# Kernel optimization log

Measured on AMD Instinct MI355X. Metric: run time of the kernel, lower is better.

The kernel has to match this reference:

```python
import jax, jax.numpy as jnp
import numpy as np

H = 16
MAX_LEN = 150
NEG_INF = -1e30  # stand-in for -inf that is fp16-safe after cast; matches masked_fill(-inf) semantics


def setup_inputs() -> dict:
    key = jax.random.key(0)
    ks = jax.random.split(key, 12)
    B, L, D = 4, 1024, 1024
    Dh = D // H
    Q = jax.random.normal(ks[0], (B, L, D), jnp.float32)
    K = jax.random.normal(ks[1], (B, L, D), jnp.float32)
    V = jax.random.normal(ks[2], (B, L, D), jnp.float32)
    # boolean mask, True = masked out; keep diagonal unmasked to avoid fully-masked rows
    mask = jax.random.bernoulli(ks[3], 0.3, (B, L, L))
    mask = jnp.logical_and(mask, ~jnp.eye(L, dtype=bool)[None])
    s = 0.02
    Wq = jax.random.normal(ks[4], (D, D), jnp.float32) * s
    Wk = jax.random.normal(ks[5], (D, D), jnp.float32) * s
    Wv = jax.random.normal(ks[6], (D, D), jnp.float32) * s
    Wo = jax.random.normal(ks[7], (D, D), jnp.float32) * s
    bq = jax.random.normal(ks[8], (D,), jnp.float32) * s
    bk = jax.random.normal(ks[9], (D,), jnp.float32) * s
    bv = jax.random.normal(ks[10], (D,), jnp.float32) * s
    bo = jax.random.normal(ks[11], (D,), jnp.float32) * s
    pos_emb = jnp.zeros((2 * MAX_LEN + 1, Dh), jnp.float32)  # nn.Parameter(torch.zeros(...))
    # perturb so the bias path is exercised
    pos_emb = pos_emb + jax.random.normal(jax.random.fold_in(key, 99), pos_emb.shape, jnp.float32) * s
    return {"Q": Q, "K": K, "V": V, "mask": mask,
            "Wq": Wq, "bq": bq, "Wk": Wk, "bk": bk, "Wv": Wv, "bv": bv,
            "Wo": Wo, "bo": bo, "pos_emb": pos_emb}


def _mha_relative(Q, K, V, mask, Wq, bq, Wk, bk, Wv, bv, Wo, bo, pos_emb):
    B, Lq, D = Q.shape
    Lk = K.shape[1]
    Dh = D // H
    # torch nn.Linear: y = x @ W.T + b
    q = (Q @ Wq.T + bq).reshape(B, Lq, H, Dh).transpose(0, 2, 1, 3)  # [B,H,Lq,Dh]
    k = (K @ Wk.T + bk).reshape(B, Lk, H, Dh).transpose(0, 2, 1, 3)
    v = (V @ Wv.T + bv).reshape(B, Lk, H, Dh).transpose(0, 2, 1, 3)
    # relative position indices, replicating torch's negative-index wraparound via mod
    rel = jnp.arange(Lk)[None, :] - jnp.arange(Lq)[:, None]
    rel = jnp.clip(rel, -MAX_LEN, MAX_LEN)
    idx = (rel + MAX_LEN - 1) % (2 * MAX_LEN + 1)  # torch pos_embedding[-1] == row 2*max_len
    Rtab = pos_emb[idx]                            # [Lq,Lk,Dh]
    Rp = jnp.einsum('bhqd,qkd->bhqk', q, Rtab)     # relative-position bias
    scores = (jnp.einsum('bhqd,bhkd->bhqk', q, k) + Rp) / jnp.sqrt(jnp.float32(Dh))
    scores = jnp.where(mask[:, None], NEG_INF, scores)
    p = jax.nn.softmax(scores, axis=-1)
    attn = jnp.einsum('bhqk,bhkd->bhqd', p, v)     # [B,H,Lq,Dh]
    attn = attn.transpose(0, 2, 1, 3).reshape(B, Lq, D)
    return attn @ Wo.T + bo                        # dropout is identity in eval


def reference(Q, K, V, mask, Wq, bq, Wk, bk, Wv, bv, Wo, bo, pos_emb):
    return _mha_relative(Q, K, V, mask, Wq, bq, Wk, bk, Wv, bv, Wo, bo, pos_emb)
```

## Files before the change

### kernel.cpp

```cpp
#include <hip/hip_runtime.h>
#include <hip/hip_bf16.h>

#define BB 4
#define LL 1024
#define DD 1024
#define HH 16
#define DH 64
#define NPOS 301
#define MAXL 150
#define NEG_INF -1e30f

typedef __attribute__((ext_vector_type(4))) float f32x4;
typedef __attribute__((ext_vector_type(8))) short short8;

__device__ inline unsigned short f2b(float x) {
    __hip_bfloat16 h = __float2bfloat16(x);
    return *reinterpret_cast<unsigned short*>(&h);
}
__device__ inline unsigned pack2(float a, float b) {
    return (unsigned)f2b(a) | ((unsigned)f2b(b) << 16);
}
__device__ inline float b2f(unsigned short u) {
    return __uint_as_float((unsigned)u << 16);
}

template <bool F32>
__device__ inline short8 ld8(const void* p, size_t off) {
    if constexpr (F32) {
        const float* q = (const float*)p + off;
        float4 a = *reinterpret_cast<const float4*>(q);
        float4 b = *reinterpret_cast<const float4*>(q + 4);
        short8 r;
        r[0] = (short)f2b(a.x); r[1] = (short)f2b(a.y);
        r[2] = (short)f2b(a.z); r[3] = (short)f2b(a.w);
        r[4] = (short)f2b(b.x); r[5] = (short)f2b(b.y);
        r[6] = (short)f2b(b.z); r[7] = (short)f2b(b.w);
        return r;
    } else {
        return *reinterpret_cast<const short8*>((const unsigned short*)p + off);
    }
}

__global__ __launch_bounds__(256) void pack_mask(const int* __restrict__ mask,
                                                 unsigned long long* __restrict__ bits)
{
    const int wid = (blockIdx.x * 256 + threadIdx.x) >> 6;
    const int lane = threadIdx.x & 63;
    const int v = mask[(size_t)wid * 64 + lane];
    const unsigned long long b = __ballot(v != 0);
    if (lane == 0) bits[wid] = b;
}

template <int EPI, bool GN, bool AF32, bool WF32>
__global__ __launch_bounds__(256) void gemm_mfma(
    const void* __restrict__ A, const void* __restrict__ W,
    const float* __restrict__ bias, void* __restrict__ Cout,
    int M, int N, int K, float oscale)
{
    __shared__ alignas(16) unsigned short As[128 * 40];
    __shared__ alignas(16) unsigned short Bs[64 * 40];
    const int tid = threadIdx.x;
    const int w = tid >> 6, lane = tid & 63;
    const int wr = w >> 1, wc = w & 1;
    const int g = lane >> 4, fr = lane & 15;
    const int m0 = blockIdx.y * 128;
    const int n0 = blockIdx.x * 64;

    f32x4 acc[4][2];
#pragma unroll
    for (int i = 0; i < 4; ++i)
#pragma unroll
        for (int j = 0; j < 2; ++j) acc[i][j] = (f32x4){0.f, 0.f, 0.f, 0.f};

    const int arow0 = tid >> 2, agg = tid & 3;
    for (int k0 = 0; k0 < K; k0 += 32) {
        {
            short8 v0 = ld8<AF32>(A, (size_t)(m0 + arow0) * K + k0 + agg * 8);
            short8 v1 = ld8<AF32>(A, (size_t)(m0 + arow0 + 64) * K + k0 + agg * 8);
            int nr = n0 + arow0;
            if (GN && nr >= N) nr = N - 1;
            short8 bv = ld8<WF32>(W, (size_t)nr * K + k0 + agg * 8);
            *reinterpret_cast<short8*>(&As[arow0 * 40 + agg * 8]) = v0;
            *reinterpret_cast<short8*>(&As[(arow0 + 64) * 40 + agg * 8]) = v1;
            *reinterpret_cast<short8*>(&Bs[arow0 * 40 + agg * 8]) = bv;
        }
        __syncthreads();
        short8 af[4], bf[2];
#pragma unroll
        for (int i = 0; i < 4; ++i)
            af[i] = *reinterpret_cast<const short8*>(
                &As[(wr * 64 + i * 16 + fr) * 40 + g * 8]);
#pragma unroll
        for (int j = 0; j < 2; ++j)
            bf[j] = *reinterpret_cast<const short8*>(
                &Bs[(wc * 32 + j * 16 + fr) * 40 + g * 8]);
#pragma unroll
        for (int i = 0; i < 4; ++i)
#pragma unroll
            for (int j = 0; j < 2; ++j)
                acc[i][j] = __builtin_amdgcn_mfma_f32_16x16x32_bf16(
                    af[i], bf[j], acc[i][j], 0, 0, 0);
        __syncthreads();
    }

#pragma unroll
    for (int i = 0; i < 4; ++i) {
#pragma unroll
        for (int j = 0; j < 2; ++j) {
#pragma unroll
            for (int r = 0; r < 4; ++r) {
                const int row = m0 + wr * 64 + i * 16 + g * 4 + r;
                const int col = n0 + wc * 32 + j * 16 + fr;
                if (GN && col >= N) continue;
                const float val = (acc[i][j][r] + (bias ? bias[col] : 0.f)) * oscale;
                if (EPI == 0) {
                    ((float*)Cout)[(size_t)row * N + col] = val;
                } else if (EPI == 1) {
                    const int b = row >> 10, l = row & 1023, hh = col >> 6, dh = col & 63;
                    ((unsigned short*)Cout)[(((size_t)(b * HH + hh)) * LL + l) * DH + dh] = f2b(val);
                } else if (EPI == 2) {
                    const int b = row >> 10, l = row & 1023, hh = col >> 6, dh = col & 63;
                    ((unsigned short*)Cout)[(((size_t)(b * HH + hh)) * DH + dh) * LL + l] = f2b(val);
                } else {
                    ((unsigned short*)Cout)[(size_t)row * N + col] = f2b(val);
                }
            }
        }
    }
}

__global__ __launch_bounds__(256) void attn_mfma(
    const unsigned short* __restrict__ qbf,
    const unsigned short* __restrict__ kbf,
    const unsigned short* __restrict__ vT,
    const unsigned short* __restrict__ qpos,
    const unsigned long long* __restrict__ mbits,
    unsigned short* __restrict__ outb)
{
    const int bh = blockIdx.x;
    const int qblk = blockIdx.y;
    const int b = bh >> 4, h = bh & 15;
    const int tid = threadIdx.x;
    const int w = tid >> 6;
    const int qh = w & 1;
    const int kh = w >> 1;
    const int lane = tid & 63;
    const int g = lane >> 4;
    const int qc = lane & 15;
    const int gq = qblk * 32 + qh * 16 + qc;
    const int ql = qh * 16 + qc;

    __shared__ alignas(16) unsigned char Plds[4 * 2048];
    __shared__ alignas(16) unsigned short Qp[32 * NPOS];
    float* Mrg = (float*)Qp;
    unsigned char* myP = Plds + w * 2048 + qc * 128;
    const int swz = (qc & 7) << 4;

    {
        const unsigned short* qslab = qpos + ((size_t)bh * LL + (size_t)qblk * 32) * NPOS;
        for (int i = tid; i < (32 * NPOS) / 8; i += 256)
            *reinterpret_cast<short8*>(&Qp[i * 8]) =
                *reinterpret_cast<const short8*>(qslab + (size_t)i * 8);
    }

    const unsigned short* qrow = qbf + ((size_t)bh * LL + gq) * DH;
    const short8 qf0 = *reinterpret_cast<const short8*>(qrow + g * 8);
    const short8 qf1 = *reinterpret_cast<const short8*>(qrow + g * 8 + 32);

    const unsigned short* kb0 = kbf + (size_t)bh * LL * DH;
    const unsigned short* vb0 = vT + (size_t)bh * DH * LL;
    const unsigned long long* mwp = mbits + ((size_t)b * LL + gq) * (LL / 64);
    const unsigned short* qpr = &Qp[ql * NPOS];

    float mrun = -3.0e38f, lrun = 0.f;
    f32x4 o[4];
#pragma unroll
    for (int m = 0; m < 4; ++m) o[m] = (f32x4){0.f, 0.f, 0.f, 0.f};

    __syncthreads();
    const float c_left = b2f(qpr[300]);
    const float c_right = b2f(qpr[299]);

    for (int it = 0; it < 8; ++it) {
        const int kt = kh * 64 + it * 128;

        f32x4 s[4];
#pragma unroll
        for (int m = 0; m < 4; ++m) s[m] = (f32x4){0.f, 0.f, 0.f, 0.f};
#pragma unroll
        for (int m = 0; m < 4; ++m) {
            const unsigned short* krow = kb0 + (size_t)(kt + m * 16 + qc) * DH + g * 8;
            short8 a0 = *reinterpret_cast<const short8*>(krow);
            short8 a1 = *reinterpret_cast<const short8*>(krow + 32);
            s[m] = __builtin_amdgcn_mfma_f32_16x16x32_bf16(a0, qf0, s[m], 0, 0, 0);
            s[m] = __builtin_amdgcn_mfma_f32_16x16x32_bf16(a1, qf1, s[m], 0, 0, 0);
        }

        const unsigned long long mw = mwp[kt >> 6];
        float tmax = -3.0e38f;
#pragma unroll
        for (int m = 0; m < 4; ++m) {
            const int kb = kt + m * 16 + g * 4;
            const unsigned msub = (unsigned)(mw >> (m * 16 + g * 4)) & 0xFu;
            const int p0 = kb - gq + 149;
            float rp0, rp1, rp2, rp3;
            if (p0 > 299) {
                rp0 = rp1 = rp2 = rp3 = c_right;
            } else if (p0 < -3) {
                rp0 = rp1 = rp2 = rp3 = c_left;
            } else if (p0 >= 0 && p0 <= 296) {
                rp0 = b2f(qpr[p0]);     rp1 = b2f(qpr[p0 + 1]);
                rp2 = b2f(qpr[p0 + 2]); rp3 = b2f(qpr[p0 + 3]);
            } else {
                int i0 = p0 < 0 ? 300 : p0;
                int i1 = p0 + 1 < 0 ? 300 : (p0 + 1 > 299 ? 299 : p0 + 1);
                int i2 = p0 + 2 < 0 ? 300 : (p0 + 2 > 299 ? 299 : p0 + 2);
                int i3 = p0 + 3 > 299 ? 299 : p0 + 3;
                rp0 = b2f(qpr[i0]); rp1 = b2f(qpr[i1]);
                rp2 = b2f(qpr[i2]); rp3 = b2f(qpr[i3]);
            }
#pragma unroll
            for (int r = 0; r < 4; ++r) {
                const float rp = (r == 0 ? rp0 : r == 1 ? rp1 : r == 2 ? rp2 : rp3);
                float x = s[m][r] + rp;
                x = (msub >> r) & 1 ? NEG_INF : x;
                s[m][r] = x;
                tmax = fmaxf(tmax, x);
            }
        }

        tmax = fmaxf(tmax, __shfl_xor(tmax, 16));
        tmax = fmaxf(tmax, __shfl_xor(tmax, 32));
        const float nm = fmaxf(mrun, tmax);
        const float al = __expf(mrun - nm);
        mrun = nm;
        float ls = 0.f;
#pragma unroll
        for (int m = 0; m < 4; ++m)
#pragma unroll
            for (int r = 0; r < 4; ++r) {
                const float p = __expf(s[m][r] - nm);
                s[m][r] = p;
                ls += p;
            }
        ls += __shfl_xor(ls, 16);
        ls += __shfl_xor(ls, 32);
        lrun = lrun * al + ls;
#pragma unroll
        for (int m = 0; m < 4; ++m) o[m] *= al;

#pragma unroll
        for (int m = 0; m < 4; ++m) {
            *reinterpret_cast<unsigned*>(myP + ((32 * m + 8 * g) ^ swz)) = pack2(s[m][0], s[m][1]);
            *reinterpret_cast<unsigned*>(myP + ((32 * m + 8 * g + 4) ^ swz)) = pack2(s[m][2], s[m][3]);
        }
        const short8 pf0 = *reinterpret_cast<const short8*>(myP + ((16 * g) ^ swz));
        const short8 pf1 = *reinterpret_cast<const short8*>(myP + ((64 + 16 * g) ^ swz));

#pragma unroll
        for (int m = 0; m < 4; ++m) {
            const unsigned short* vrow = vb0 + (size_t)(m * 16 + qc) * LL + kt + g * 8;
            short8 va0 = *reinterpret_cast<const short8*>(vrow);
            short8 va1 = *reinterpret_cast<const short8*>(vrow + 32);
            o[m] = __builtin_amdgcn_mfma_f32_16x16x32_bf16(va0, pf0, o[m], 0, 0, 0);
            o[m] = __builtin_amdgcn_mfma_f32_16x16x32_bf16(va1, pf1, o[m], 0, 0, 0);
        }
    }

    __syncthreads();
    if (kh == 1) {
        float* d = Mrg + ((size_t)qh * 64 + lane) * 18;
#pragma unroll
        for (int m = 0; m < 4; ++m)
#pragma unroll
            for (int r = 0; r < 4; ++r) d[m * 4 + r] = o[m][r];
        d[16] = mrun; d[17] = lrun;
    }
    __syncthreads();
    if (kh == 0) {
        const float* d = Mrg + ((size_t)qh * 64 + lane) * 18;
        const float m1 = d[16], l1 = d[17];
        const float M = fmaxf(mrun, m1);
        const float a0 = __expf(mrun - M), a1 = __expf(m1 - M);
        const float linv = 1.f / (lrun * a0 + l1 * a1);
        unsigned short* orow = outb + ((size_t)b * LL + gq) * DD + h * DH;
#pragma unroll
        for (int m = 0; m < 4; ++m) {
            ushort4 st;
            st.x = f2b((o[m][0] * a0 + d[m * 4 + 0] * a1) * linv);
            st.y = f2b((o[m][1] * a0 + d[m * 4 + 1] * a1) * linv);
            st.z = f2b((o[m][2] * a0 + d[m * 4 + 2] * a1) * linv);
            st.w = f2b((o[m][3] * a0 + d[m * 4 + 3] * a1) * linv);
            *reinterpret_cast<ushort4*>(orow + m * 16 + g * 4) = st;
        }
    }
}

extern "C" void kernel_launch(void* const* d_in, const int* in_sizes, int n_in,
                              void* d_out, int out_size, void* d_ws, size_t ws_size,
                              hipStream_t stream)
{
    const float* Q  = (const float*)d_in[0];
    const float* K  = (const float*)d_in[1];
    const float* V  = (const float*)d_in[2];
    const int* mask = (const int*)d_in[3];
    const float* Wq = (const float*)d_in[4];
    const float* bq = (const float*)d_in[5];
    const float* Wk = (const float*)d_in[6];
    const float* bk = (const float*)d_in[7];
    const float* Wv = (const float*)d_in[8];
    const float* bv = (const float*)d_in[9];
    const float* Wo = (const float*)d_in[10];
    const float* bo = (const float*)d_in[11];
    const float* pe = (const float*)d_in[12];
    float* out = (float*)d_out;

    unsigned short* ws = (unsigned short*)d_ws;
    const size_t NQ = (size_t)BB * HH * LL * DH;
    unsigned short* qbf = ws;
    unsigned short* kbf = qbf + NQ;
    unsigned short* vT  = kbf + NQ;
    unsigned short* attnb = vT + NQ;
    unsigned short* qpos = attnb + NQ;
    unsigned long long* mbits =
        (unsigned long long*)(qpos + (size_t)BB * HH * LL * NPOS);

    const dim3 blk(256);
    const int M = BB * LL;

    pack_mask<<<dim3((BB * LL * LL / 64) * 64 / 256), blk, 0, stream>>>(mask, mbits);
    gemm_mfma<1, false, true, true><<<dim3(16, 32), blk, 0, stream>>>(
        Q, Wq, bq, qbf, M, DD, DD, 0.125f);
    gemm_mfma<1, false, true, true><<<dim3(16, 32), blk, 0, stream>>>(
        K, Wk, bk, kbf, M, DD, DD, 1.0f);
    gemm_mfma<2, false, true, true><<<dim3(16, 32), blk, 0, stream>>>(
        V, Wv, bv, vT, M, DD, DD, 1.0f);
    gemm_mfma<3, true, false, true><<<dim3(5, 512), blk, 0, stream>>>(
        qbf, pe, nullptr, qpos, BB * HH * LL, NPOS, DH, 1.0f);
    attn_mfma<<<dim3(BB * HH, LL / 32), dim3(256), 0, stream>>>(
        qbf, kbf, vT, qpos, mbits, attnb);
    gemm_mfma<0, false, false, true><<<dim3(16, 32), blk, 0, stream>>>(
        attnb, Wo, bo, out, M, DD, DD, 1.0f);
}
```

Measured before the change: 302.6 us.

## Batch Q/K/V projections into one launch and double GEMM K-tile to 64

Merges the three separate QKV projection GEMM launches into one kernel using blockIdx.z to select the input, weights, bias and output layout. It also increases the shared-memory K tile from 32 to 64, running two MFMA sub-steps per tile so each iteration needs fewer barriers and global-load rounds. The output epilogue selector becomes a runtime value instead of a template parameter. Shared memory per block grows, which may reduce occupancy.

```diff
diff --git a/kernel.cpp b/kernel.cpp
--- a/kernel.cpp
+++ b/kernel.cpp
@@ -51,20 +51,17 @@
     if (lane == 0) bits[wid] = b;
 }
 
-template <int EPI, bool GN, bool AF32, bool WF32>
-__global__ __launch_bounds__(256) void gemm_mfma(
+template <bool GN, bool AF32, bool WF32>
+__device__ __forceinline__ void gemm_body(
     const void* __restrict__ A, const void* __restrict__ W,
     const float* __restrict__ bias, void* __restrict__ Cout,
-    int M, int N, int K, float oscale)
-{
-    __shared__ alignas(16) unsigned short As[128 * 40];
-    __shared__ alignas(16) unsigned short Bs[64 * 40];
+    int M, int N, int K, float oscale, int epi,
+    int m0, int n0, unsigned short* As, unsigned short* Bs)
+{
     const int tid = threadIdx.x;
     const int w = tid >> 6, lane = tid & 63;
     const int wr = w >> 1, wc = w & 1;
     const int g = lane >> 4, fr = lane & 15;
-    const int m0 = blockIdx.y * 128;
-    const int n0 = blockIdx.x * 64;
 
     f32x4 acc[4][2];
 #pragma unroll
@@ -72,34 +69,43 @@
 #pragma unroll
         for (int j = 0; j < 2; ++j) acc[i][j] = (f32x4){0.f, 0.f, 0.f, 0.f};
 
-    const int arow0 = tid >> 2, agg = tid & 3;
-    for (int k0 = 0; k0 < K; k0 += 32) {
+    const int arow0 = tid >> 2, agg = (tid & 3) * 8;
+    for (int k0 = 0; k0 < K; k0 += 64) {
         {
-            short8 v0 = ld8<AF32>(A, (size_t)(m0 + arow0) * K + k0 + agg * 8);
-            short8 v1 = ld8<AF32>(A, (size_t)(m0 + arow0 + 64) * K + k0 + agg * 8);
+            short8 a00 = ld8<AF32>(A, (size_t)(m0 + arow0) * K + k0 + agg);
+            short8 a01 = ld8<AF32>(A, (size_t)(m0 + arow0) * K + k0 + agg + 32);
+            short8 a10 = ld8<AF32>(A, (size_t)(m0 + arow0 + 64) * K + k0 + agg);
+            short8 a11 = ld8<AF32>(A, (size_t)(m0 + arow0 + 64) * K + k0 + agg + 32);
             int nr = n0 + arow0;
             if (GN && nr >= N) nr = N - 1;
-            short8 bv = ld8<WF32>(W, (size_t)nr * K + k0 + agg * 8);
-            *reinterpret_cast<short8*>(&As[arow0 * 40 + agg * 8]) = v0;
-            *reinterpret_cast<short8*>(&As[(arow0 + 64) * 40 + agg * 8]) = v1;
-            *reinterpret_cast<short8*>(&Bs[arow0 * 40 + agg * 8]) = bv;
+            short8 b0 = ld8<WF32>(W, (size_t)nr * K + k0 + agg);
+            short8 b1 = ld8<WF32>(W, (size_t)nr * K + k0 + agg + 32);
+            *reinterpret_cast<short8*>(&As[arow0 * 72 + agg]) = a00;
+            *reinterpret_cast<short8*>(&As[arow0 * 72 + agg + 32]) = a01;
+            *reinterpret_cast<short8*>(&As[(arow0 + 64) * 72 + agg]) = a10;
+            *reinterpret_cast<short8*>(&As[(arow0 + 64) * 72 + agg + 32]) = a11;
+            *reinterpret_cast<short8*>(&Bs[arow0 * 72 + agg]) = b0;
+            *reinterpret_cast<short8*>(&Bs[arow0 * 72 + agg + 32]) = b1;
         }
         __syncthreads();
-        short8 af[4], bf[2];
-#pragma unroll
-        for (int i = 0; i < 4; ++i)
-            af[i] = *reinterpret_cast<const short8*>(
-                &As[(wr * 64 + i * 16 + fr) * 40 + g * 8]);
-#pragma unroll
-        for (int j = 0; j < 2; ++j)
-            bf[j] = *reinterpret_cast<const short8*>(
-                &Bs[(wc * 32 + j * 16 + fr) * 40 + g * 8]);
-#pragma unroll
-        for (int i = 0; i < 4; ++i)
+#pragma unroll
+        for (int kk = 0; kk < 2; ++kk) {
+            short8 af[4], bf[2];
+#pragma unroll
+            for (int i = 0; i < 4; ++i)
+                af[i] = *reinterpret_cast<const short8*>(
+                    &As[(wr * 64 + i * 16 + fr) * 72 + kk * 32 + g * 8]);
 #pragma unroll
             for (int j = 0; j < 2; ++j)
-                acc[i][j] = __builtin_amdgcn_mfma_f32_16x16x32_bf16(
-                    af[i], bf[j], acc[i][j], 0, 0, 0);
+                bf[j] = *reinterpret_cast<const short8*>(
+                    &Bs[(wc * 32 + j * 16 + fr) * 72 + kk * 32 + g * 8]);
+#pragma unroll
+            for (int i = 0; i < 4; ++i)
+#pragma unroll
+                for (int j = 0; j < 2; ++j)
+                    acc[i][j] = __builtin_amdgcn_mfma_f32_16x16x32_bf16(
+                        af[i], bf[j], acc[i][j], 0, 0, 0);
+        }
         __syncthreads();
     }
 
@@ -113,12 +119,12 @@
                 const int col = n0 + wc * 32 + j * 16 + fr;
                 if (GN && col >= N) continue;
                 const float val = (acc[i][j][r] + (bias ? bias[col] : 0.f)) * oscale;
-                if (EPI == 0) {
+                if (epi == 0) {
                     ((float*)Cout)[(size_t)row * N + col] = val;
-                } else if (EPI == 1) {
+                } else if (epi == 1) {
                     const int b = row >> 10, l = row & 1023, hh = col >> 6, dh = col & 63;
                     ((unsigned short*)Cout)[(((size_t)(b * HH + hh)) * LL + l) * DH + dh] = f2b(val);
-                } else if (EPI == 2) {
+                } else if (epi == 2) {
                     const int b = row >> 10, l = row & 1023, hh = col >> 6, dh = col & 63;
                     ((unsigned short*)Cout)[(((size_t)(b * HH + hh)) * DH + dh) * LL + l] = f2b(val);
                 } else {
@@ -127,6 +133,41 @@
             }
         }
     }
+}
+
+template <int EPI, bool GN, bool AF32, bool WF32>
+__global__ __launch_bounds__(256) void gemm_mfma(
+    const void* __restrict__ A, const void* __restrict__ W,
+    const float* __restrict__ bias, void* __restrict__ Cout,
+    int M, int N, int K, float oscale)
+{
+    __shared__ alignas(16) unsigned short As[128 * 72];
+    __shared__ alignas(16) unsigned short Bs[64 * 72];
+    gemm_body<GN, AF32, WF32>(A, W, bias, Cout, M, N, K, oscale, EPI,
+                              blockIdx.y * 128, blockIdx.x * 64, As, Bs);
+}
+
+__global__ __launch_bounds__(256) void gemm_qkv(
+    const float* __restrict__ Q, const float* __restrict__ K,
+    const float* __restrict__ V,
+    const float* __restrict__ Wq, const float* __restrict__ Wk,
+    const float* __restrict__ Wv,
+    const float* __restrict__ bq, const float* __restrict__ bk,
+    const float* __restrict__ bv,
+    unsigned short* __restrict__ qbf, unsigned short* __restrict__ kbf,
+    unsigned short* __restrict__ vT)
+{
+    __shared__ alignas(16) unsigned short As[128 * 72];
+    __shared__ alignas(16) unsigned short Bs[64 * 72];
+    const int z = blockIdx.z;
+    const float* A = (z == 0) ? Q : (z == 1) ? K : V;
+    const float* W = (z == 0) ? Wq : (z == 1) ? Wk : Wv;
+    const float* bias = (z == 0) ? bq : (z == 1) ? bk : bv;
+    void* Cout = (z == 0) ? (void*)qbf : (z == 1) ? (void*)kbf : (void*)vT;
+    const int epi = (z == 2) ? 2 : 1;
+    const float oscale = (z == 0) ? 0.125f : 1.0f;
+    gemm_body<false, true, true>(A, W, bias, Cout, BB * LL, DD, DD, oscale, epi,
+                                 blockIdx.y * 128, blockIdx.x * 64, As, Bs);
 }
 
 __global__ __launch_bounds__(256) void attn_mfma(
@@ -329,12 +370,8 @@
     const int M = BB * LL;
 
     pack_mask<<<dim3((BB * LL * LL / 64) * 64 / 256), blk, 0, stream>>>(mask, mbits);
-    gemm_mfma<1, false, true, true><<<dim3(16, 32), blk, 0, stream>>>(
-        Q, Wq, bq, qbf, M, DD, DD, 0.125f);
-    gemm_mfma<1, false, true, true><<<dim3(16, 32), blk, 0, stream>>>(
-        K, Wk, bk, kbf, M, DD, DD, 1.0f);
-    gemm_mfma<2, false, true, true><<<dim3(16, 32), blk, 0, stream>>>(
-        V, Wv, bv, vT, M, DD, DD, 1.0f);
+    gemm_qkv<<<dim3(16, 32, 3), blk, 0, stream>>>(
+        Q, K, V, Wq, Wk, Wv, bq, bk, bv, qbf, kbf, vT);
     gemm_mfma<3, true, false, true><<<dim3(5, 512), blk, 0, stream>>>(
         qbf, pe, nullptr, qpos, BB * HH * LL, NPOS, DH, 1.0f);
     attn_mfma<<<dim3(BB * HH, LL / 32), dim3(256), 0, stream>>>(
```

Measured after the change: 295.3 us. 1.02x faster.
